# Kernel optimization log

Hardware: AMD Instinct MI355X
Metric: run time of the kernel (lower is better)

The kernel has to match this reference:

```python
import jax, jax.numpy as jnp
import numpy as np

T, B = 256, 64
X_DIM, H_DIM, Z_DIM = 128, 1024, 128


def _lin(k, out_d, in_d):
    return jax.random.normal(k, (out_d, in_d), jnp.float32) * 0.05


def setup_inputs() -> dict:
    key = jax.random.key(0)
    ks = jax.random.split(key, 18)
    return {
        "x": jax.random.normal(ks[0], (T, B, X_DIM), jnp.float32),
        "y": jax.random.uniform(ks[1], (T, B, X_DIM), jnp.float32),
        "eps": jax.random.normal(ks[2], (T, B, Z_DIM), jnp.float32),
        # hidden_state_rnn: GRU(x_dim -> h_dim), bias=False
        "h_Wih": _lin(ks[3], 3 * H_DIM, X_DIM),
        "h_Whh": _lin(ks[4], 3 * H_DIM, H_DIM),
        # rnn: GRU(h_dim + x_dim -> h_dim), bias=False (input is [y_t, h_t])
        "a_Wih": _lin(ks[5], 3 * H_DIM, X_DIM + H_DIM),
        "a_Whh": _lin(ks[6], 3 * H_DIM, H_DIM),
        "enc_W1": _lin(ks[7], H_DIM, H_DIM), "enc_b1": jnp.zeros(H_DIM, jnp.float32),
        "enc_W2": _lin(ks[8], H_DIM, H_DIM), "enc_b2": jnp.zeros(H_DIM, jnp.float32),
        "encm_W": _lin(ks[9], Z_DIM, H_DIM), "encm_b": jnp.zeros(Z_DIM, jnp.float32),
        "encs_W": _lin(ks[10], Z_DIM, H_DIM), "encs_b": jnp.zeros(Z_DIM, jnp.float32),
        "pr_W": _lin(ks[11], H_DIM, H_DIM), "pr_b": jnp.zeros(H_DIM, jnp.float32),
        "prm_W": _lin(ks[12], Z_DIM, H_DIM), "prm_b": jnp.zeros(Z_DIM, jnp.float32),
        "prs_W": _lin(ks[13], Z_DIM, H_DIM), "prs_b": jnp.zeros(Z_DIM, jnp.float32),
        "dec_W1": _lin(ks[14], H_DIM, H_DIM + Z_DIM), "dec_b1": jnp.zeros(H_DIM, jnp.float32),
        "dec_W2": _lin(ks[15], H_DIM, H_DIM), "dec_b2": jnp.zeros(H_DIM, jnp.float32),
        "decm_W": _lin(ks[16], X_DIM, H_DIM), "decm_b": jnp.zeros(X_DIM, jnp.float32),
        "decs_W": _lin(ks[17], X_DIM, H_DIM), "decs_b": jnp.zeros(X_DIM, jnp.float32),
    }


def _gru(xs, Wih, Whh):
    """Single-layer PyTorch-style GRU without biases. xs: [T,B,in]. Returns [T,B,H]."""
    h0 = jnp.zeros((xs.shape[1], Whh.shape[1]), xs.dtype)
    def step(h, xt):
        gi = xt @ Wih.T                      # [B, 3H]
        gh = h @ Whh.T                       # [B, 3H]
        ir, iz, inn = jnp.split(gi, 3, axis=-1)
        hr, hz, hn = jnp.split(gh, 3, axis=-1)
        r = jax.nn.sigmoid(ir + hr)
        zg = jax.nn.sigmoid(iz + hz)
        n = jnp.tanh(inn + r * hn)
        h_new = (1.0 - zg) * n + zg * h
        return h_new, h_new
    return jax.lax.scan(step, h0, xs)[1]


def srnn_forward(x, y, eps, h_Wih, h_Whh, a_Wih, a_Whh,
                 enc_W1, enc_b1, enc_W2, enc_b2, encm_W, encm_b, encs_W, encs_b,
                 pr_W, pr_b, prm_W, prm_b, prs_W, prs_b,
                 dec_W1, dec_b1, dec_W2, dec_b2, decm_W, decm_b, decs_W, decs_b):
    h_seq = _gru(x, h_Wih, h_Whh)            # [T,B,H] forward-time states
    # NOTE: original code aliases h_list and reverses it in place, so all later
    # uses of h_list[t] actually see the time-reversed sequence. Reproduce that.
    h_rev = h_seq[::-1]
    y_rev = y[::-1]
    a_rev = _gru(jnp.concatenate([y_rev, h_rev], axis=-1), a_Wih, a_Whh)  # backward GRU
    a_fwd = a_rev[::-1]                      # a at forward time t saw steps t..T-1

    enc = jax.nn.relu(jax.nn.relu(a_fwd @ enc_W1.T + enc_b1) @ enc_W2.T + enc_b2)
    enc_mean = enc @ encm_W.T + encm_b       # [T,B,Z]
    enc_std = jax.nn.softplus(enc @ encs_W.T + encs_b)
    z = eps * enc_std + enc_mean             # reparameterized sample

    pri = jax.nn.relu(h_rev @ pr_W.T + pr_b)  # bug-faithful: reversed h
    prior_mean = pri @ prm_W.T + prm_b
    prior_std = jax.nn.softplus(pri @ prs_W.T + prs_b)

    dec = jax.nn.relu(
        jax.nn.relu(jnp.concatenate([z, h_rev], axis=-1) @ dec_W1.T + dec_b1)
        @ dec_W2.T + dec_b2)
    dec_mean = jax.nn.sigmoid(dec @ decm_W.T + decm_b)  # [T,B,X]
    dec_std = jax.nn.softplus(dec @ decs_W.T + decs_b)

    kld = 0.5 * jnp.sum(
        2.0 * jnp.log(prior_std) - 2.0 * jnp.log(enc_std)
        + (enc_std ** 2 + (enc_mean - prior_mean) ** 2) / prior_std ** 2 - 1.0)
    nll = -jnp.sum(y * jnp.log(dec_mean) + (1.0 - y) * jnp.log(1.0 - dec_mean))
    return kld, nll, enc_mean, enc_std, dec_mean, dec_std


def reference(x, y, eps, h_Wih, h_Whh, a_Wih, a_Whh,
              enc_W1, enc_b1, enc_W2, enc_b2, encm_W, encm_b, encs_W, encs_b,
              pr_W, pr_b, prm_W, prm_b, prs_W, prs_b,
              dec_W1, dec_b1, dec_W2, dec_b2, decm_W, decm_b, decs_W, decs_b):
    return srnn_forward(x, y, eps, h_Wih, h_Whh, a_Wih, a_Whh,
                        enc_W1, enc_b1, enc_W2, enc_b2, encm_W, encm_b, encs_W, encs_b,
                        pr_W, pr_b, prm_W, prm_b, prs_W, prs_b,
                        dec_W1, dec_b1, dec_W2, dec_b2, decm_W, decm_b, decs_W, decs_b)
```

## Files before the change

### kernel.cpp

```cpp
#include <hip/hip_runtime.h>
#include <cstdint>
#include <cstddef>

#define NT   256
#define NB   64
#define XD   128
#define HD   1024
#define ZD   128
#define H3   3072
#define TBM  16384

typedef __attribute__((ext_vector_type(8))) short bf16x8;
typedef __attribute__((ext_vector_type(4))) float f32x4;
typedef __attribute__((ext_vector_type(4))) unsigned int u32x4;

__device__ __forceinline__ unsigned short f2bf(float f){
  unsigned int u = __float_as_uint(f);
  u += 0x7fffu + ((u >> 16) & 1u);
  return (unsigned short)(u >> 16);
}
__device__ __forceinline__ float bf2f(unsigned short h){
  return __uint_as_float(((unsigned int)h) << 16);
}

template<int N>
__device__ __forceinline__ void vwait(){
  asm volatile("s_waitcnt vmcnt(%0)" :: "i"(N) : "memory");
  __builtin_amdgcn_sched_barrier(0);
}

__device__ __forceinline__ float fsigmoid(float x){
  return 1.f / (1.f + __expf(-x));
}
__device__ __forceinline__ float ftanh(float x){
  float xc = fminf(fmaxf(x, -15.f), 15.f);
  float e = __expf(2.f * xc);
  return (e - 1.f) / (e + 1.f);
}

__device__ __forceinline__ void wait_tags(const unsigned int* tags, unsigned int target){
  if (threadIdx.x < 64){
    const unsigned int* p = tags + threadIdx.x * 32;
    for (;;){
      unsigned int v;
      asm volatile("global_load_dword %0, %1, off sc0 sc1\n\ts_waitcnt vmcnt(0)"
                   : "=v"(v) : "v"(p) : "memory");
      if (__all((int)(v >= target))) break;
      __builtin_amdgcn_s_sleep(2);
    }
  }
  __syncthreads();
}

__global__ void cvt_bf16(const float* __restrict__ src, unsigned short* __restrict__ dst, int n){
  for (int i = blockIdx.x*blockDim.x + threadIdx.x; i < n; i += gridDim.x*blockDim.x)
    dst[i] = f2bf(src[i]);
}

template<int ACT, int OUT_BF, int BIAS>
__launch_bounds__(256)
__global__ void gemm_bf16(const unsigned short* __restrict__ A1, int rev1, int K1,
                          const unsigned short* __restrict__ A2, int rev2, int K,
                          const unsigned short* __restrict__ W,
                          const float* __restrict__ bias,
                          void* __restrict__ Cv, int N, int m0)
{
  __shared__ __align__(16) unsigned short As[128][40];
  __shared__ __align__(16) unsigned short Ws[128][40];
  const int tid   = threadIdx.x;
  const int mbase = blockIdx.y * 128;
  const int nbase = blockIdx.x * 128;
  const int wid = tid >> 6, lane = tid & 63;
  const int wr = wid >> 1, wc = wid & 1;
  const int fr = lane & 15;
  const int kc = (lane >> 4) * 8;
  const int K2 = K - K1;
  const int nk = K >> 5;

  f32x4 acc[4][4];
  #pragma unroll
  for (int i = 0; i < 4; ++i)
    #pragma unroll
    for (int j = 0; j < 4; ++j)
      acc[i][j] = (f32x4){0.f, 0.f, 0.f, 0.f};

  for (int ks = 0; ks < nk; ++ks){
    const int k0 = ks << 5;
    __syncthreads();
    for (int l = tid; l < 512; l += 256){
      int row = l >> 2, c = l & 3;
      int kk = k0 + c*8;
      int m = m0 + mbase + row;
      uint4 v;
      if (kk < K1){
        int mm = rev1 ? (((255 - (m >> 6)) << 6) | (m & 63)) : m;
        v = *(const uint4*)(A1 + (size_t)mm * K1 + kk);
      } else {
        int mm = rev2 ? (((255 - (m >> 6)) << 6) | (m & 63)) : m;
        v = *(const uint4*)(A2 + (size_t)mm * K2 + (kk - K1));
      }
      *(uint4*)&As[row][c*8] = v;
    }
    for (int l = tid; l < 512; l += 256){
      int row = l >> 2, c = l & 3;
      uint4 v = *(const uint4*)(W + (size_t)(nbase + row) * K + k0 + c*8);
      *(uint4*)&Ws[row][c*8] = v;
    }
    __syncthreads();
    bf16x8 af[4], bfm[4];
    #pragma unroll
    for (int f = 0; f < 4; ++f) af[f]  = *(const bf16x8*)&As[wr*64 + f*16 + fr][kc];
    #pragma unroll
    for (int f = 0; f < 4; ++f) bfm[f] = *(const bf16x8*)&Ws[wc*64 + f*16 + fr][kc];
    #pragma unroll
    for (int i = 0; i < 4; ++i)
      #pragma unroll
      for (int j = 0; j < 4; ++j)
        acc[i][j] = __builtin_amdgcn_mfma_f32_16x16x32_bf16(af[i], bfm[j], acc[i][j], 0, 0, 0);
  }

  #pragma unroll
  for (int i = 0; i < 4; ++i){
    #pragma unroll
    for (int j = 0; j < 4; ++j){
      #pragma unroll
      for (int r = 0; r < 4; ++r){
        int row = mbase + wr*64 + i*16 + (lane >> 4)*4 + r;
        int col = nbase + wc*64 + j*16 + fr;
        float v = acc[i][j][r];
        if (BIAS) v += bias[col];
        if (ACT == 1) v = fmaxf(v, 0.f);
        else if (ACT == 2) v = 1.f / (1.f + expf(-v));
        else if (ACT == 3) v = (v > 20.f) ? v : log1pf(expf(v));
        if (OUT_BF) ((unsigned short*)Cv)[(size_t)row * N + col] = f2bf(v);
        else        ((float*)Cv)[(size_t)row * N + col] = v;
      }
    }
  }
}

__global__ __launch_bounds__(256, 1)
void gru_seq(const unsigned short* __restrict__ W3,
             const unsigned short* __restrict__ gi,
             unsigned short* __restrict__ seq,
             float* __restrict__ hstate,
             unsigned int* __restrict__ tags,
             int t0, int dir, int out_off, int nsteps)
{
  __shared__ __align__(16) uint4 Wf[32][3][64];
  __shared__ __align__(16) unsigned short hb2[64][16];
  const int tid  = threadIdx.x;
  const int bid  = blockIdx.x;
  const int c0   = bid * 16;
  const int wid  = tid >> 6, lane = tid & 63;
  const int fr   = lane & 15, q = lane >> 4;
  const int rowb = wid*16 + q*4;
  const int arow = wid*16 + fr;

  for (int ks = wid*8; ks < wid*8 + 8; ++ks)
    #pragma unroll
    for (int g = 0; g < 3; ++g)
      Wf[ks][g][lane] = *(const uint4*)(W3 + (size_t)(g*HD + c0 + fr)*HD + ks*32 + q*8);

  float hc[4];
  if (t0 == 0){
    hc[0] = hc[1] = hc[2] = hc[3] = 0.f;
  } else {
    #pragma unroll
    for (int r = 0; r < 4; ++r)
      hc[r] = hstate[(size_t)(rowb + r)*HD + c0 + fr];
  }
  __syncthreads();

  for (int tt = 0; tt < nsteps; ++tt){
    const int t = t0 + tt;

    unsigned short g_ir[4], g_iz[4], g_in[4];
    {
      const unsigned short* gb = gi + (size_t)tt*NB*H3;
      #pragma unroll
      for (int r = 0; r < 4; ++r){
        const unsigned short* p = gb + (size_t)(rowb + r)*H3 + c0 + fr;
        g_ir[r] = p[0];
        g_iz[r] = p[HD];
        g_in[r] = p[2*HD];
      }
    }

    f32x4 aR = (f32x4){0.f,0.f,0.f,0.f};
    f32x4 aZ = (f32x4){0.f,0.f,0.f,0.f};
    f32x4 aN = (f32x4){0.f,0.f,0.f,0.f};

    if (t > 0){
      if (tt >= 1) wait_tags(tags, (unsigned int)tt);
      const unsigned short* hp = seq + (size_t)(out_off + dir*(t-1))*NB*HD
                                     + (size_t)arow*HD + q*8;
      u32x4 A[32];
      #pragma unroll
      for (int ks = 0; ks < 32; ++ks)
        asm volatile("global_load_dwordx4 %0, %1, off offset:%2"
                     : "=v"(A[ks]) : "v"(hp), "i"(ks*64));
      #pragma unroll
      for (int b4 = 0; b4 < 4; ++b4){
        if (b4 == 0) vwait<24>();
        else if (b4 == 1) vwait<16>();
        else if (b4 == 2) vwait<8>();
        else vwait<0>();
        #pragma unroll
        for (int k8 = 0; k8 < 8; ++k8){
          const int ks = b4*8 + k8;
          bf16x8 a = *(const bf16x8*)&A[ks];
          aR = __builtin_amdgcn_mfma_f32_16x16x32_bf16(a, *(const bf16x8*)&Wf[ks][0][lane], aR, 0, 0, 0);
          aZ = __builtin_amdgcn_mfma_f32_16x16x32_bf16(a, *(const bf16x8*)&Wf[ks][1][lane], aZ, 0, 0, 0);
          aN = __builtin_amdgcn_mfma_f32_16x16x32_bf16(a, *(const bf16x8*)&Wf[ks][2][lane], aN, 0, 0, 0);
        }
      }
    }

    #pragma unroll
    for (int r = 0; r < 4; ++r){
      float rr = fsigmoid(bf2f(g_ir[r]) + aR[r]);
      float zz = fsigmoid(bf2f(g_iz[r]) + aZ[r]);
      float nn = ftanh(bf2f(g_in[r]) + rr * aN[r]);
      hc[r] = (1.f - zz) * nn + zz * hc[r];
      hb2[rowb + r][fr] = f2bf(hc[r]);
    }
    __syncthreads();
    {
      int row = tid >> 2, c4 = (tid & 3) * 4;
      unsigned long long v = *(const unsigned long long*)&hb2[row][c4];
      unsigned long long* dst = (unsigned long long*)(seq + (size_t)(out_off + dir*t)*NB*HD
                                                          + (size_t)row*HD + c0 + c4);
      (void)__hip_atomic_exchange(dst, v, __ATOMIC_RELAXED, __HIP_MEMORY_SCOPE_AGENT);
    }
    if (tt < nsteps - 1){
      vwait<0>();
      __syncthreads();
      if (tid == 0)
        (void)__hip_atomic_exchange(tags + bid*32, (unsigned int)(tt + 1),
                                    __ATOMIC_RELAXED, __HIP_MEMORY_SCOPE_AGENT);
    }
  }

  #pragma unroll
  for (int r = 0; r < 4; ++r)
    hstate[(size_t)(rowb + r)*HD + c0 + fr] = hc[r];
}

__global__ void z_make(const float* __restrict__ eps, const float* __restrict__ em,
                       const float* __restrict__ es, unsigned short* __restrict__ zb, int n){
  for (int i = blockIdx.x*blockDim.x + threadIdx.x; i < n; i += gridDim.x*blockDim.x)
    zb[i] = f2bf(eps[i] * es[i] + em[i]);
}

__global__ void kld_partial(const float* __restrict__ em, const float* __restrict__ es,
                            const float* __restrict__ pm, const float* __restrict__ ps,
                            float* __restrict__ part, int n){
  float s = 0.f;
  for (int i = blockIdx.x*blockDim.x + threadIdx.x; i < n; i += gridDim.x*blockDim.x){
    float e = es[i], p = ps[i], d = em[i] - pm[i];
    s += 2.f*(logf(p) - logf(e)) + (e*e + d*d)/(p*p) - 1.f;
  }
  __shared__ float red[256];
  red[threadIdx.x] = s; __syncthreads();
  for (int off = 128; off; off >>= 1){
    if (threadIdx.x < off) red[threadIdx.x] += red[threadIdx.x + off];
    __syncthreads();
  }
  if (threadIdx.x == 0) part[blockIdx.x] = red[0];
}

__global__ void nll_partial(const float* __restrict__ y, const float* __restrict__ dm,
                            float* __restrict__ part, int n){
  float s = 0.f;
  for (int i = blockIdx.x*blockDim.x + threadIdx.x; i < n; i += gridDim.x*blockDim.x){
    float yy = y[i], d = dm[i];
    s += yy * logf(d) + (1.f - yy) * logf(1.f - d);
  }
  __shared__ float red[256];
  red[threadIdx.x] = s; __syncthreads();
  for (int off = 128; off; off >>= 1){
    if (threadIdx.x < off) red[threadIdx.x] += red[threadIdx.x + off];
    __syncthreads();
  }
  if (threadIdx.x == 0) part[blockIdx.x] = red[0];
}

__global__ void final_sum(const float* __restrict__ part, int n, float scale, float* __restrict__ out){
  float s = 0.f;
  for (int i = threadIdx.x; i < n; i += 256) s += part[i];
  __shared__ float red[256];
  red[threadIdx.x] = s; __syncthreads();
  for (int off = 128; off; off >>= 1){
    if (threadIdx.x < off) red[threadIdx.x] += red[threadIdx.x + off];
    __syncthreads();
  }
  if (threadIdx.x == 0) out[0] = scale * red[0];
}

extern "C" void kernel_launch(void* const* d_in, const int* in_sizes, int n_in,
                              void* d_out, int out_size, void* d_ws, size_t ws_size,
                              hipStream_t stream)
{
  const float* x   = (const float*)d_in[0];
  const float* y   = (const float*)d_in[1];
  const float* eps = (const float*)d_in[2];
  const float* enc_b1 = (const float*)d_in[8];
  const float* enc_b2 = (const float*)d_in[10];
  const float* encm_b = (const float*)d_in[12];
  const float* encs_b = (const float*)d_in[14];
  const float* pr_b   = (const float*)d_in[16];
  const float* prm_b  = (const float*)d_in[18];
  const float* prs_b  = (const float*)d_in[20];
  const float* dec_b1 = (const float*)d_in[22];
  const float* dec_b2 = (const float*)d_in[24];
  const float* decm_b = (const float*)d_in[26];
  const float* decs_b = (const float*)d_in[28];

  char* ws = (char*)d_ws;
  size_t off = 0;
  auto alloc = [&](size_t bytes){ size_t o = off; off += (bytes + 255) & ~(size_t)255; return o; };
  const size_t o_big   = alloc((size_t)71303168);
  const size_t o_hseq  = alloc((size_t)TBM * HD * 2);
  const size_t o_aseq  = alloc((size_t)TBM * HD * 2);
  const size_t o_wbf   = alloc((size_t)16384000 * 2);
  const size_t o_hst   = alloc((size_t)NB * HD * 4);
  const size_t o_bar   = alloc((size_t)32768);
  const size_t o_pkld  = alloc((size_t)1024 * 4);
  const size_t o_pnll  = alloc((size_t)1024 * 4);
  (void)off; (void)ws_size;

  char* big = ws + o_big;
  unsigned short* gih = (unsigned short*)(big);
  unsigned short* xbf = (unsigned short*)(big + 50331648);
  unsigned short* ybf = (unsigned short*)(big + 54525952);
  unsigned short* tA  = (unsigned short*)(big);
  unsigned short* tB  = (unsigned short*)(big + 33554432);
  unsigned short* zbf = (unsigned short*)(big + 67108864);

  unsigned short* hseq = (unsigned short*)(ws + o_hseq);
  unsigned short* aseq = (unsigned short*)(ws + o_aseq);
  unsigned short* wbf  = (unsigned short*)(ws + o_wbf);
  float* hstate = (float*)(ws + o_hst);
  unsigned int* bar = (unsigned int*)(ws + o_bar);
  float* pkld = (float*)(ws + o_pkld);
  float* pnll = (float*)(ws + o_pnll);

  const int   widx[15] = {3,4,5,6,7,9,11,13,15,17,19,21,23,25,27};
  const size_t wsz[15] = {393216,3145728,3538944,3145728,1048576,1048576,131072,131072,
                          1048576,131072,131072,1179648,1048576,131072,131072};
  size_t woff[15]; { size_t a = 0; for (int i = 0; i < 15; ++i){ woff[i] = a; a += wsz[i]; } }
  unsigned short* w_hWih = wbf + woff[0];
  unsigned short* w_hWhh = wbf + woff[1];
  unsigned short* w_aWih = wbf + woff[2];
  unsigned short* w_aWhh = wbf + woff[3];
  unsigned short* w_enc1 = wbf + woff[4];
  unsigned short* w_enc2 = wbf + woff[5];
  unsigned short* w_encm = wbf + woff[6];
  unsigned short* w_encs = wbf + woff[7];
  unsigned short* w_pr   = wbf + woff[8];
  unsigned short* w_prm  = wbf + woff[9];
  unsigned short* w_prs  = wbf + woff[10];
  unsigned short* w_dec1 = wbf + woff[11];
  unsigned short* w_dec2 = wbf + woff[12];
  unsigned short* w_decm = wbf + woff[13];
  unsigned short* w_decs = wbf + woff[14];

  float* out = (float*)d_out;
  float* em_out = out + 2;
  float* es_out = out + 2 + 2097152;
  float* dm_out = out + 2 + 2*2097152;
  float* ds_out = out + 2 + 3*2097152;
  float* pm = dm_out;
  float* ps = ds_out;

  cvt_bf16<<<256, 256, 0, stream>>>(x, xbf, TBM*XD);
  cvt_bf16<<<256, 256, 0, stream>>>(y, ybf, TBM*XD);
  for (int i = 0; i < 15; ++i)
    cvt_bf16<<<256, 256, 0, stream>>>((const float*)d_in[widx[i]], wbf + woff[i], (int)wsz[i]);
  (void)hipMemsetAsync(bar, 0, 32768, stream);

  const dim3 blk(256);
  const dim3 gHalf3072(H3/128, 64);
  const dim3 g1024(HD/128, TBM/128);
  const dim3 g128(1, TBM/128);

  for (int c = 0; c < 2; ++c){
    gemm_bf16<0,1,0><<<gHalf3072, blk, 0, stream>>>(xbf, 0, XD, (const unsigned short*)nullptr, 0, XD,
                                                    w_hWih, nullptr, gih, H3, c*8192);
    gru_seq<<<64, 256, 0, stream>>>(w_hWhh, gih, hseq, hstate, bar + c*2048,
                                    c*128, +1, 0, 128);
  }

  for (int c = 0; c < 2; ++c){
    gemm_bf16<0,1,0><<<gHalf3072, blk, 0, stream>>>(ybf, 1, XD, hseq, 1, XD + HD,
                                                    w_aWih, nullptr, gih, H3, c*8192);
    gru_seq<<<64, 256, 0, stream>>>(w_aWhh, gih, aseq, hstate, bar + (2 + c)*2048,
                                    c*128, -1, 255, 128);
  }

  gemm_bf16<1,1,1><<<g1024, blk, 0, stream>>>(aseq, 0, HD, (const unsigned short*)nullptr, 0, HD,
                                              w_enc1, enc_b1, tA, HD, 0);
  gemm_bf16<1,1,1><<<g1024, blk, 0, stream>>>(tA, 0, HD, (const unsigned short*)nullptr, 0, HD,
                                              w_enc2, enc_b2, tB, HD, 0);
  gemm_bf16<0,0,1><<<g128, blk, 0, stream>>>(tB, 0, HD, (const unsigned short*)nullptr, 0, HD,
                                             w_encm, encm_b, em_out, ZD, 0);
  gemm_bf16<3,0,1><<<g128, blk, 0, stream>>>(tB, 0, HD, (const unsigned short*)nullptr, 0, HD,
                                             w_encs, encs_b, es_out, ZD, 0);
  z_make<<<2048, 256, 0, stream>>>(eps, em_out, es_out, zbf, TBM*ZD);

  gemm_bf16<1,1,1><<<g1024, blk, 0, stream>>>(hseq, 1, HD, (const unsigned short*)nullptr, 1, HD,
                                              w_pr, pr_b, tA, HD, 0);
  gemm_bf16<0,0,1><<<g128, blk, 0, stream>>>(tA, 0, HD, (const unsigned short*)nullptr, 0, HD,
                                             w_prm, prm_b, pm, ZD, 0);
  gemm_bf16<3,0,1><<<g128, blk, 0, stream>>>(tA, 0, HD, (const unsigned short*)nullptr, 0, HD,
                                             w_prs, prs_b, ps, ZD, 0);
  kld_partial<<<1024, 256, 0, stream>>>(em_out, es_out, pm, ps, pkld, TBM*ZD);
  final_sum<<<1, 256, 0, stream>>>(pkld, 1024, 0.5f, out + 0);

  gemm_bf16<1,1,1><<<g1024, blk, 0, stream>>>(zbf, 0, ZD, hseq, 1, ZD + HD,
                                              w_dec1, dec_b1, tA, HD, 0);
  gemm_bf16<1,1,1><<<g1024, blk, 0, stream>>>(tA, 0, HD, (const unsigned short*)nullptr, 0, HD,
                                              w_dec2, dec_b2, tB, HD, 0);
  gemm_bf16<2,0,1><<<g128, blk, 0, stream>>>(tB, 0, HD, (const unsigned short*)nullptr, 0, HD,
                                             w_decm, decm_b, dm_out, ZD, 0);
  gemm_bf16<3,0,1><<<g128, blk, 0, stream>>>(tB, 0, HD, (const unsigned short*)nullptr, 0, HD,
                                             w_decs, decs_b, ds_out, ZD, 0);

  nll_partial<<<1024, 256, 0, stream>>>(y, dm_out, pnll, TBM*XD);
  final_sum<<<1, 256, 0, stream>>>(pnll, 1024, -1.0f, out + 1);
}
```

Measured before the change: 4.820 ms.

## Overlap next-chunk GRU input GEMM with recurrent steps in one fat kernel

Splits each GRU sequence into four 64-step chunks and launches a combined kernel where 64 blocks run the recurrent steps while the other 192 blocks compute the input-projection GEMM for the next chunk into a second buffer. This hides the per-chunk input GEMM behind the latency-bound recurrence. It also merges all fp32-to-bf16 conversions into a single vectorised kernel, removes the sleep in the spin-wait, and replaces the per-step block barrier before the tag publish with a shared-memory counter so the last wave publishes. The extra blocks compete for memory bandwidth and L2 with the recurrent blocks, and more kernel launches are needed.

```diff
diff --git a/kernel.cpp b/kernel.cpp
--- a/kernel.cpp
+++ b/kernel.cpp
@@ -46,15 +46,44 @@
       asm volatile("global_load_dword %0, %1, off sc0 sc1\n\ts_waitcnt vmcnt(0)"
                    : "=v"(v) : "v"(p) : "memory");
       if (__all((int)(v >= target))) break;
-      __builtin_amdgcn_s_sleep(2);
     }
   }
   __syncthreads();
 }
 
-__global__ void cvt_bf16(const float* __restrict__ src, unsigned short* __restrict__ dst, int n){
-  for (int i = blockIdx.x*blockDim.x + threadIdx.x; i < n; i += gridDim.x*blockDim.x)
-    dst[i] = f2bf(src[i]);
+struct CvtArgs { const float* src[17]; };
+
+__global__ void cvt_all(CvtArgs a, unsigned short* wdst, unsigned short* xdst, unsigned short* ydst){
+  const long NG = 2572288;
+  for (long g = blockIdx.x*blockDim.x + threadIdx.x; g < NG; g += (long)gridDim.x*blockDim.x){
+    long i = g * 8;
+    const float* s; unsigned short* d;
+    if      (i < 393216)  { s=a.src[0]+i;             d=wdst+i; }
+    else if (i < 3538944) { s=a.src[1]+(i-393216);    d=wdst+i; }
+    else if (i < 7077888) { s=a.src[2]+(i-3538944);   d=wdst+i; }
+    else if (i < 10223616){ s=a.src[3]+(i-7077888);   d=wdst+i; }
+    else if (i < 11272192){ s=a.src[4]+(i-10223616);  d=wdst+i; }
+    else if (i < 12320768){ s=a.src[5]+(i-11272192);  d=wdst+i; }
+    else if (i < 12451840){ s=a.src[6]+(i-12320768);  d=wdst+i; }
+    else if (i < 12582912){ s=a.src[7]+(i-12451840);  d=wdst+i; }
+    else if (i < 13631488){ s=a.src[8]+(i-12582912);  d=wdst+i; }
+    else if (i < 13762560){ s=a.src[9]+(i-13631488);  d=wdst+i; }
+    else if (i < 13893632){ s=a.src[10]+(i-13762560); d=wdst+i; }
+    else if (i < 15073280){ s=a.src[11]+(i-13893632); d=wdst+i; }
+    else if (i < 16121856){ s=a.src[12]+(i-15073280); d=wdst+i; }
+    else if (i < 16252928){ s=a.src[13]+(i-16121856); d=wdst+i; }
+    else if (i < 16384000){ s=a.src[14]+(i-16252928); d=wdst+i; }
+    else if (i < 18481152){ s=a.src[15]+(i-16384000); d=xdst+(i-16384000); }
+    else                  { s=a.src[16]+(i-18481152); d=ydst+(i-18481152); }
+    float4 v0 = *(const float4*)s;
+    float4 v1 = *(const float4*)(s + 4);
+    u32x4 o;
+    o.x = (unsigned int)f2bf(v0.x) | ((unsigned int)f2bf(v0.y) << 16);
+    o.y = (unsigned int)f2bf(v0.z) | ((unsigned int)f2bf(v0.w) << 16);
+    o.z = (unsigned int)f2bf(v1.x) | ((unsigned int)f2bf(v1.y) << 16);
+    o.w = (unsigned int)f2bf(v1.z) | ((unsigned int)f2bf(v1.w) << 16);
+    *(u32x4*)d = o;
+  }
 }
 
 template<int ACT, int OUT_BF, int BIAS>
@@ -139,16 +168,92 @@
   }
 }
 
-__global__ __launch_bounds__(256, 1)
-void gru_seq(const unsigned short* __restrict__ W3,
-             const unsigned short* __restrict__ gi,
-             unsigned short* __restrict__ seq,
-             float* __restrict__ hstate,
-             unsigned int* __restrict__ tags,
-             int t0, int dir, int out_off, int nsteps)
+__device__ void gemm_gi_tile(char* smem,
+                             const unsigned short* __restrict__ A1, int rev1, int K1,
+                             const unsigned short* __restrict__ A2, int rev2, int K,
+                             const unsigned short* __restrict__ W,
+                             unsigned short* __restrict__ C, int m0, int bx, int by)
 {
-  __shared__ __align__(16) uint4 Wf[32][3][64];
-  __shared__ __align__(16) unsigned short hb2[64][16];
+  unsigned short (*As)[40] = (unsigned short(*)[40])smem;
+  unsigned short (*Ws)[40] = (unsigned short(*)[40])(smem + 10240);
+  const int tid   = threadIdx.x;
+  const int mbase = by * 128;
+  const int nbase = bx * 128;
+  const int wid = tid >> 6, lane = tid & 63;
+  const int wr = wid >> 1, wc = wid & 1;
+  const int fr = lane & 15;
+  const int kc = (lane >> 4) * 8;
+  const int K2 = K - K1;
+  const int nk = K >> 5;
+
+  f32x4 acc[4][4];
+  #pragma unroll
+  for (int i = 0; i < 4; ++i)
+    #pragma unroll
+    for (int j = 0; j < 4; ++j)
+      acc[i][j] = (f32x4){0.f, 0.f, 0.f, 0.f};
+
+  for (int ks = 0; ks < nk; ++ks){
+    const int k0 = ks << 5;
+    __syncthreads();
+    for (int l = tid; l < 512; l += 256){
+      int row = l >> 2, c = l & 3;
+      int kk = k0 + c*8;
+      int m = m0 + mbase + row;
+      uint4 v;
+      if (kk < K1){
+        int mm = rev1 ? (((255 - (m >> 6)) << 6) | (m & 63)) : m;
+        v = *(const uint4*)(A1 + (size_t)mm * K1 + kk);
+      } else {
+        int mm = rev2 ? (((255 - (m >> 6)) << 6) | (m & 63)) : m;
+        v = *(const uint4*)(A2 + (size_t)mm * K2 + (kk - K1));
+      }
+      *(uint4*)&As[row][c*8] = v;
+    }
+    for (int l = tid; l < 512; l += 256){
+      int row = l >> 2, c = l & 3;
+      uint4 v = *(const uint4*)(W + (size_t)(nbase + row) * K + k0 + c*8);
+      *(uint4*)&Ws[row][c*8] = v;
+    }
+    __syncthreads();
+    bf16x8 af[4], bfm[4];
+    #pragma unroll
+    for (int f = 0; f < 4; ++f) af[f]  = *(const bf16x8*)&As[wr*64 + f*16 + fr][kc];
+    #pragma unroll
+    for (int f = 0; f < 4; ++f) bfm[f] = *(const bf16x8*)&Ws[wc*64 + f*16 + fr][kc];
+    #pragma unroll
+    for (int i = 0; i < 4; ++i)
+      #pragma unroll
+      for (int j = 0; j < 4; ++j)
+        acc[i][j] = __builtin_amdgcn_mfma_f32_16x16x32_bf16(af[i], bfm[j], acc[i][j], 0, 0, 0);
+  }
+
+  #pragma unroll
+  for (int i = 0; i < 4; ++i){
+    #pragma unroll
+    for (int j = 0; j < 4; ++j){
+      #pragma unroll
+      for (int r = 0; r < 4; ++r){
+        int row = mbase + wr*64 + i*16 + (lane >> 4)*4 + r;
+        int col = nbase + wc*64 + j*16 + fr;
+        C[(size_t)row * H3 + col] = f2bf(acc[i][j][r]);
+      }
+    }
+  }
+  __syncthreads();
+}
+
+__device__ void gru_body(char* smem,
+                         const unsigned short* __restrict__ W3,
+                         const unsigned short* __restrict__ gi,
+                         unsigned short* __restrict__ seq,
+                         float* __restrict__ hstate,
+                         unsigned int* __restrict__ tags,
+                         int t0, int dir, int out_off, int nsteps)
+{
+  uint4 (*Wf)[3][64] = (uint4(*)[3][64])smem;
+  unsigned short (*hb2)[16] = (unsigned short(*)[16])(smem + 98304);
+  unsigned int* scnt = (unsigned int*)(smem + 100352);
   const int tid  = threadIdx.x;
   const int bid  = blockIdx.x;
   const int c0   = bid * 16;
@@ -161,6 +266,7 @@
     #pragma unroll
     for (int g = 0; g < 3; ++g)
       Wf[ks][g][lane] = *(const uint4*)(W3 + (size_t)(g*HD + c0 + fr)*HD + ks*32 + q*8);
+  if (tid == 0) *scnt = 0u;
 
   float hc[4];
   if (t0 == 0){
@@ -235,16 +341,44 @@
     }
     if (tt < nsteps - 1){
       vwait<0>();
-      __syncthreads();
-      if (tid == 0)
-        (void)__hip_atomic_exchange(tags + bid*32, (unsigned int)(tt + 1),
-                                    __ATOMIC_RELAXED, __HIP_MEMORY_SCOPE_AGENT);
+      if (lane == 0){
+        unsigned int old = atomicAdd(scnt, 1u);
+        if (old == (unsigned int)(4*tt + 3))
+          (void)__hip_atomic_exchange(tags + bid*32, (unsigned int)(tt + 1),
+                                      __ATOMIC_RELAXED, __HIP_MEMORY_SCOPE_AGENT);
+      }
     }
   }
 
   #pragma unroll
   for (int r = 0; r < 4; ++r)
     hstate[(size_t)(rowb + r)*HD + c0 + fr] = hc[r];
+}
+
+__global__ __launch_bounds__(256, 1)
+void gru_seq(const unsigned short* __restrict__ W3, const unsigned short* __restrict__ gi,
+             unsigned short* __restrict__ seq, float* __restrict__ hstate,
+             unsigned int* __restrict__ tags, int t0, int dir, int out_off, int nsteps)
+{
+  __shared__ __align__(16) char smem[100608];
+  gru_body(smem, W3, gi, seq, hstate, tags, t0, dir, out_off, nsteps);
+}
+
+__global__ __launch_bounds__(256, 1)
+void gru_fat(const unsigned short* __restrict__ W3, const unsigned short* __restrict__ gi,
+             unsigned short* __restrict__ seq, float* __restrict__ hstate,
+             unsigned int* __restrict__ tags, int t0, int dir, int out_off, int nsteps,
+             const unsigned short* __restrict__ gA1, int grev1, int gK1,
+             const unsigned short* __restrict__ gA2, int grev2, int gK,
+             const unsigned short* __restrict__ gW, unsigned short* __restrict__ gC, int gm0)
+{
+  __shared__ __align__(16) char smem[100608];
+  if (blockIdx.x < 64){
+    gru_body(smem, W3, gi, seq, hstate, tags, t0, dir, out_off, nsteps);
+  } else {
+    for (int tl = blockIdx.x - 64; tl < 768; tl += 192)
+      gemm_gi_tile(smem, gA1, grev1, gK1, gA2, grev2, gK, gW, gC, gm0, tl % 24, tl / 24);
+  }
 }
 
 __global__ void z_make(const float* __restrict__ eps, const float* __restrict__ em,
@@ -302,7 +436,6 @@
                               void* d_out, int out_size, void* d_ws, size_t ws_size,
                               hipStream_t stream)
 {
-  const float* x   = (const float*)d_in[0];
   const float* y   = (const float*)d_in[1];
   const float* eps = (const float*)d_in[2];
   const float* enc_b1 = (const float*)d_in[8];
@@ -325,15 +458,16 @@
   const size_t o_aseq  = alloc((size_t)TBM * HD * 2);
   const size_t o_wbf   = alloc((size_t)16384000 * 2);
   const size_t o_hst   = alloc((size_t)NB * HD * 4);
-  const size_t o_bar   = alloc((size_t)32768);
+  const size_t o_bar   = alloc((size_t)65536);
   const size_t o_pkld  = alloc((size_t)1024 * 4);
   const size_t o_pnll  = alloc((size_t)1024 * 4);
   (void)off; (void)ws_size;
 
   char* big = ws + o_big;
-  unsigned short* gih = (unsigned short*)(big);
-  unsigned short* xbf = (unsigned short*)(big + 50331648);
-  unsigned short* ybf = (unsigned short*)(big + 54525952);
+  unsigned short* gihA = (unsigned short*)(big);
+  unsigned short* gihB = (unsigned short*)(big + 25165824);
+  unsigned short* xbf  = (unsigned short*)(big + 50331648);
+  unsigned short* ybf  = (unsigned short*)(big + 54525952);
   unsigned short* tA  = (unsigned short*)(big);
   unsigned short* tB  = (unsigned short*)(big + 33554432);
   unsigned short* zbf = (unsigned short*)(big + 67108864);
@@ -346,7 +480,7 @@
   float* pkld = (float*)(ws + o_pkld);
   float* pnll = (float*)(ws + o_pnll);
 
-  const int   widx[15] = {3,4,5,6,7,9,11,13,15,17,19,21,23,25,27};
+  const int widx[15] = {3,4,5,6,7,9,11,13,15,17,19,21,23,25,27};
   const size_t wsz[15] = {393216,3145728,3538944,3145728,1048576,1048576,131072,131072,
                           1048576,131072,131072,1179648,1048576,131072,131072};
   size_t woff[15]; { size_t a = 0; for (int i = 0; i < 15; ++i){ woff[i] = a; a += wsz[i]; } }
@@ -374,58 +508,53 @@
   float* pm = dm_out;
   float* ps = ds_out;
 
-  cvt_bf16<<<256, 256, 0, stream>>>(x, xbf, TBM*XD);
-  cvt_bf16<<<256, 256, 0, stream>>>(y, ybf, TBM*XD);
-  for (int i = 0; i < 15; ++i)
-    cvt_bf16<<<256, 256, 0, stream>>>((const float*)d_in[widx[i]], wbf + woff[i], (int)wsz[i]);
-  (void)hipMemsetAsync(bar, 0, 32768, stream);
+  CvtArgs ca;
+  for (int i = 0; i < 15; ++i) ca.src[i] = (const float*)d_in[widx[i]];
+  ca.src[15] = (const float*)d_in[0];
+  ca.src[16] = (const float*)d_in[1];
+  cvt_all<<<2048, 256, 0, stream>>>(ca, wbf, xbf, ybf);
+  (void)hipMemsetAsync(bar, 0, 65536, stream);
 
   const dim3 blk(256);
-  const dim3 gHalf3072(H3/128, 64);
+  const dim3 gQ3072(24, 32);
   const dim3 g1024(HD/128, TBM/128);
   const dim3 g128(1, TBM/128);
-
-  for (int c = 0; c < 2; ++c){
-    gemm_bf16<0,1,0><<<gHalf3072, blk, 0, stream>>>(xbf, 0, XD, (const unsigned short*)nullptr, 0, XD,
-                                                    w_hWih, nullptr, gih, H3, c*8192);
-    gru_seq<<<64, 256, 0, stream>>>(w_hWhh, gih, hseq, hstate, bar + c*2048,
-                                    c*128, +1, 0, 128);
-  }
-
-  for (int c = 0; c < 2; ++c){
-    gemm_bf16<0,1,0><<<gHalf3072, blk, 0, stream>>>(ybf, 1, XD, hseq, 1, XD + HD,
-                                                    w_aWih, nullptr, gih, H3, c*8192);
-    gru_seq<<<64, 256, 0, stream>>>(w_aWhh, gih, aseq, hstate, bar + (2 + c)*2048,
-                                    c*128, -1, 255, 128);
-  }
-
-  gemm_bf16<1,1,1><<<g1024, blk, 0, stream>>>(aseq, 0, HD, (const unsigned short*)nullptr, 0, HD,
-                                              w_enc1, enc_b1, tA, HD, 0);
-  gemm_bf16<1,1,1><<<g1024, blk, 0, stream>>>(tA, 0, HD, (const unsigned short*)nullptr, 0, HD,
-                                              w_enc2, enc_b2, tB, HD, 0);
-  gemm_bf16<0,0,1><<<g128, blk, 0, stream>>>(tB, 0, HD, (const unsigned short*)nullptr, 0, HD,
-                                             w_encm, encm_b, em_out, ZD, 0);
-  gemm_bf16<3,0,1><<<g128, blk, 0, stream>>>(tB, 0, HD, (const unsigned short*)nullptr, 0, HD,
-                                             w_encs, encs_b, es_out, ZD, 0);
+  const unsigned short* nul = (const unsigned short*)nullptr;
+
+  gemm_bf16<0,1,0><<<gQ3072, blk, 0, stream>>>(xbf, 0, XD, nul, 0, XD, w_hWih, nullptr, gihA, H3, 0);
+  gru_fat<<<256, blk, 0, stream>>>(w_hWhh, gihA, hseq, hstate, bar + 0*2048, 0,   +1, 0, 64,
+                                   xbf, 0, XD, nul, 0, XD, w_hWih, gihB, 4096);
+  gru_fat<<<256, blk, 0, stream>>>(w_hWhh, gihB, hseq, hstate, bar + 1*2048, 64,  +1, 0, 64,
+                                   xbf, 0, XD, nul, 0, XD, w_hWih, gihA, 8192);
+  gru_fat<<<256, blk, 0, stream>>>(w_hWhh, gihA, hseq, hstate, bar + 2*2048, 128, +1, 0, 64,
+                                   xbf, 0, XD, nul, 0, XD, w_hWih, gihB, 12288);
+  gru_seq<<<64, blk, 0, stream>>>(w_hWhh, gihB, hseq, hstate, bar + 3*2048, 192, +1, 0, 64);
+
+  gemm_bf16<0,1,0><<<gQ3072, blk, 0, stream>>>(ybf, 1, XD, hseq, 1, XD + HD, w_aWih, nullptr, gihA, H3, 0);
+  gru_fat<<<256, blk, 0, stream>>>(w_aWhh, gihA, aseq, hstate, bar + 4*2048, 0,   -1, 255, 64,
+                                   ybf, 1, XD, hseq, 1, XD + HD, w_aWih, gihB, 4096);
+  gru_fat<<<256, blk, 0, stream>>>(w_aWhh, gihB, aseq, hstate, bar + 5*2048, 64,  -1, 255, 64,
+                                   ybf, 1, XD, hseq, 1, XD + HD, w_aWih, gihA, 8192);
+  gru_fat<<<256, blk, 0, stream>>>(w_aWhh, gihA, aseq, hstate, bar + 6*2048, 128, -1, 255, 64,
+                                   ybf, 1, XD, hseq, 1, XD + HD, w_aWih, gihB, 12288);
+  gru_seq<<<64, blk, 0, stream>>>(w_aWhh, gihB, aseq, hstate, bar + 7*2048, 192, -1, 255, 64);
+
+  gemm_bf16<1,1,1><<<g1024, blk, 0, stream>>>(aseq, 0, HD, nul, 0, HD, w_enc1, enc_b1, tA, HD, 0);
+  gemm_bf16<1,1,1><<<g1024, blk, 0, stream>>>(tA, 0, HD, nul, 0, HD, w_enc2, enc_b2, tB, HD, 0);
+  gemm_bf16<0,0,1><<<g128, blk, 0, stream>>>(tB, 0, HD, nul, 0, HD, w_encm, encm_b, em_out, ZD, 0);
+  gemm_bf16<3,0,1><<<g128, blk, 0, stream>>>(tB, 0, HD, nul, 0, HD, w_encs, encs_b, es_out, ZD, 0);
   z_make<<<2048, 256, 0, stream>>>(eps, em_out, es_out, zbf, TBM*ZD);
 
-  gemm_bf16<1,1,1><<<g1024, blk, 0, stream>>>(hseq, 1, HD, (const unsigned short*)nullptr, 1, HD,
-                                              w_pr, pr_b, tA, HD, 0);
-  gemm_bf16<0,0,1><<<g128, blk, 0, stream>>>(tA, 0, HD, (const unsigned short*)nullptr, 0, HD,
-                                             w_prm, prm_b, pm, ZD, 0);
-  gemm_bf16<3,0,1><<<g128, blk, 0, stream>>>(tA, 0, HD, (const unsigned short*)nullptr, 0, HD,
-                                             w_prs, prs_b, ps, ZD, 0);
+  gemm_bf16<1,1,1><<<g1024, blk, 0, stream>>>(hseq, 1, HD, nul, 1, HD, w_pr, pr_b, tA, HD, 0);
+  gemm_bf16<0,0,1><<<g128, blk, 0, stream>>>(tA, 0, HD, nul, 0, HD, w_prm, prm_b, pm, ZD, 0);
+  gemm_bf16<3,0,1><<<g128, blk, 0, stream>>>(tA, 0, HD, nul, 0, HD, w_prs, prs_b, ps, ZD, 0);
   kld_partial<<<1024, 256, 0, stream>>>(em_out, es_out, pm, ps, pkld, TBM*ZD);
   final_sum<<<1, 256, 0, stream>>>(pkld, 1024, 0.5f, out + 0);
 
-  gemm_bf16<1,1,1><<<g1024, blk, 0, stream>>>(zbf, 0, ZD, hseq, 1, ZD + HD,
-                                              w_dec1, dec_b1, tA, HD, 0);
-  gemm_bf16<1,1,1><<<g1024, blk, 0, stream>>>(tA, 0, HD, (const unsigned short*)nullptr, 0, HD,
-                                              w_dec2, dec_b2, tB, HD, 0);
-  gemm_bf16<2,0,1><<<g128, blk, 0, stream>>>(tB, 0, HD, (const unsigned short*)nullptr, 0, HD,
-                                             w_decm, decm_b, dm_out, ZD, 0);
-  gemm_bf16<3,0,1><<<g128, blk, 0, stream>>>(tB, 0, HD, (const unsigned short*)nullptr, 0, HD,
-                                             w_decs, decs_b, ds_out, ZD, 0);
+  gemm_bf16<1,1,1><<<g1024, blk, 0, stream>>>(zbf, 0, ZD, hseq, 1, ZD + HD, w_dec1, dec_b1, tA, HD, 0);
+  gemm_bf16<1,1,1><<<g1024, blk, 0, stream>>>(tA, 0, HD, nul, 0, HD, w_dec2, dec_b2, tB, HD, 0);
+  gemm_bf16<2,0,1><<<g128, blk, 0, stream>>>(tB, 0, HD, nul, 0, HD, w_decm, decm_b, dm_out, ZD, 0);
+  gemm_bf16<3,0,1><<<g128, blk, 0, stream>>>(tB, 0, HD, nul, 0, HD, w_decs, decs_b, ds_out, ZD, 0);
 
   nll_partial<<<1024, 256, 0, stream>>>(y, dm_out, pnll, TBM*XD);
   final_sum<<<1, 256, 0, stream>>>(pnll, 1024, -1.0f, out + 1);
```

Result: no change. 4.839 ms (+0.4%).
